# Kernel tuning notes

Measured on AMD Instinct MI355X. Metric: run time of the kernel, lower is better.

Reference implementation:

```python
import jax, jax.numpy as jnp
import numpy as np

N_HEADS = 16

def _apply_rope(x, cos, sin):
    # x: [B, S, H, D]; cos/sin: [S, D//2]
    B, S, H, D = x.shape
    half = D // 2
    x1, x2 = x[..., :half], x[..., half:]
    c = cos[:S, None, :]  # [S, 1, half] -> broadcast over heads
    s = sin[:S, None, :]
    o1 = x1 * c - x2 * s
    o2 = x1 * s + x2 * c
    return jnp.concatenate([o1, o2], axis=-1).astype(x.dtype)


def setup_inputs() -> dict:
    key = jax.random.key(0)
    ks = jax.random.split(key, 6)
    B, S, dim = 2, 2048, 2048
    head_dim = dim // N_HEADS
    half = head_dim // 2
    x = jax.random.normal(ks[0], (B, S, dim), dtype=jnp.float32)
    # real RoPE tables (theta=10000)
    inv_freq = 1.0 / (10000.0 ** (np.arange(0, half, dtype=np.float32) / half))
    t = np.arange(S, dtype=np.float32)
    freqs = np.outer(t, inv_freq)  # [S, half]
    cos = jnp.asarray(np.cos(freqs), dtype=jnp.float32)
    sin = jnp.asarray(np.sin(freqs), dtype=jnp.float32)
    scale = 0.02
    wq = jax.random.normal(ks[1], (dim, dim), dtype=jnp.float32) * scale
    wk = jax.random.normal(ks[2], (dim, dim), dtype=jnp.float32) * scale
    wv = jax.random.normal(ks[3], (dim, dim), dtype=jnp.float32) * scale
    wo = jax.random.normal(ks[4], (dim, dim), dtype=jnp.float32) * scale
    return {"x": x, "cos": cos, "sin": sin, "wq": wq, "wk": wk, "wv": wv, "wo": wo}


def reference(x, cos, sin, wq, wk, wv, wo):
    B, S, dim = x.shape
    H = N_HEADS
    Dh = dim // H
    # QKV projections (nn.Linear: x @ W.T)
    q = (x @ wq.T).reshape(B, S, H, Dh)
    k = (x @ wk.T).reshape(B, S, H, Dh)
    v = (x @ wv.T).reshape(B, S, H, Dh)
    q = _apply_rope(q, cos, sin)
    k = _apply_rope(k, cos, sin)
    # causal attention (flash_attn_func with causal=True, dropout 0 in eval)
    scores = jnp.einsum('bqhd,bkhd->bhqk', q, k) / jnp.sqrt(jnp.asarray(Dh, x.dtype))
    causal = jnp.tril(jnp.ones((S, S), dtype=bool))
    scores = jnp.where(causal, scores, jnp.asarray(-1e30, x.dtype))
    attn = jax.nn.softmax(scores, axis=-1)
    out = jnp.einsum('bhqk,bkhd->bqhd', attn, v).reshape(B, S, dim)
    return out @ wo.T
```

## Files before the change

### kernel.cpp

```cpp
#include <hip/hip_runtime.h>

typedef short short8 __attribute__((ext_vector_type(8)));
typedef float f32x4 __attribute__((ext_vector_type(4)));
typedef unsigned short ushort_t;

__device__ __forceinline__ unsigned short f2bf(float f){
  unsigned int u = __builtin_bit_cast(unsigned int, f);
  u += 0x7FFFu + ((u >> 16) & 1u);
  return (unsigned short)(u >> 16);
}
__device__ __forceinline__ float bf2f(unsigned short u){
  return __builtin_bit_cast(float, ((unsigned int)u) << 16);
}
__device__ __forceinline__ void gload_lds16(const void* g, void* l){
  __builtin_amdgcn_global_load_lds((const __attribute__((address_space(1))) unsigned int*)g,
                                   (__attribute__((address_space(3))) unsigned int*)l, 16, 0, 0);
}

__global__ __launch_bounds__(256) void cast_bf16_kernel(const float* __restrict__ in,
                                                        ushort_t* __restrict__ out, long n4){
  long i = (long)blockIdx.x*256 + threadIdx.x;
  if (i >= n4) return;
  const float4 v = reinterpret_cast<const float4*>(in)[i];
  ushort4 o; o.x=f2bf(v.x); o.y=f2bf(v.y); o.z=f2bf(v.z); o.w=f2bf(v.w);
  reinterpret_cast<ushort4*>(out)[i] = o;
}

__global__ __launch_bounds__(256) void cast4_bf16_kernel(const float* __restrict__ w0, const float* __restrict__ w1,
                                                         const float* __restrict__ w2, const float* __restrict__ w3,
                                                         ushort_t* __restrict__ o0, ushort_t* __restrict__ o1,
                                                         ushort_t* __restrict__ o2, ushort_t* __restrict__ o3,
                                                         long n4){
  long i = (long)blockIdx.x*256 + threadIdx.x;
  if (i >= n4) return;
  const float* in; ushort_t* out;
  switch (blockIdx.y){
    case 0: in = w0; out = o0; break;
    case 1: in = w1; out = o1; break;
    case 2: in = w2; out = o2; break;
    default: in = w3; out = o3; break;
  }
  const float4 v = reinterpret_cast<const float4*>(in)[i];
  ushort4 o; o.x=f2bf(v.x); o.y=f2bf(v.y); o.z=f2bf(v.z); o.w=f2bf(v.w);
  reinterpret_cast<ushort4*>(out)[i] = o;
}

__global__ __launch_bounds__(256) void rope2_kernel(ushort_t* __restrict__ Qs,
                                                    ushort_t* __restrict__ Ks,
                                                    const float* __restrict__ cosb,
                                                    const float* __restrict__ sinb){
  long idx = (long)blockIdx.x*256 + threadIdx.x;
  ushort_t* X = blockIdx.y ? Ks : Qs;
  const float scale = blockIdx.y ? 1.0f : 0.08838834764831845f;
  int dq = (int)(idx & 15);
  long rest = idx >> 4;
  int h = (int)(rest & 15); rest >>= 4;
  int s = (int)(rest & 2047);
  int b = (int)(rest >> 11);
  long base = ((long)(b*2048 + s))*2048 + h*128;
  int d0 = dq*4;
  ushort4 x1 = *(const ushort4*)&X[base + d0];
  ushort4 x2 = *(const ushort4*)&X[base + 64 + d0];
  float4 cc = *(const float4*)&cosb[s*64 + d0];
  float4 ss = *(const float4*)&sinb[s*64 + d0];
  ushort4 o1, o2;
  { float a=bf2f(x1.x), bb=bf2f(x2.x); o1.x=f2bf((a*cc.x-bb*ss.x)*scale); o2.x=f2bf((a*ss.x+bb*cc.x)*scale); }
  { float a=bf2f(x1.y), bb=bf2f(x2.y); o1.y=f2bf((a*cc.y-bb*ss.y)*scale); o2.y=f2bf((a*ss.y+bb*cc.y)*scale); }
  { float a=bf2f(x1.z), bb=bf2f(x2.z); o1.z=f2bf((a*cc.z-bb*ss.z)*scale); o2.z=f2bf((a*ss.z+bb*cc.z)*scale); }
  { float a=bf2f(x1.w), bb=bf2f(x2.w); o1.w=f2bf((a*cc.w-bb*ss.w)*scale); o2.w=f2bf((a*ss.w+bb*cc.w)*scale); }
  *(ushort4*)&X[base + d0] = o1;
  *(ushort4*)&X[base + 64 + d0] = o2;
}


#define LDA8(P, QM) do{ \
  _Pragma("unroll") for (int i_ = 0; i_ < 4; ++i_){ \
    af[i_][0] = *(const short8*)&lA[(P)*16384 + ((QM)*128 + aRowBase + i_*16)*64 + sw0]; \
    af[i_][1] = *(const short8*)&lA[(P)*16384 + ((QM)*128 + aRowBase + i_*16)*64 + sw1]; } }while(0)

#define LDB4(P, QN) do{ \
  _Pragma("unroll") for (int j_ = 0; j_ < 2; ++j_){ \
    bfr[j_][0] = *(const short8*)&lB[(P)*16384 + ((QN)*128 + bRowBase + j_*16)*64 + sw0]; \
    bfr[j_][1] = *(const short8*)&lB[(P)*16384 + ((QN)*128 + bRowBase + j_*16)*64 + sw1]; } }while(0)

#define STAGE_A(P, QM, T) do{ \
  gload_lds16(aS0 + (long)(QM)*64*K + (long)(T)*64, &lA[(P)*16384 + (QM)*8192 + tid*8]); \
  gload_lds16(aS1 + (long)(QM)*64*K + (long)(T)*64, &lA[(P)*16384 + (QM)*8192 + 4096 + tid*8]); }while(0)

#define STAGE_B(P, QN, T) do{ \
  gload_lds16(bS0 + (long)(QN)*32*K + (long)(T)*64, &lB[(P)*16384 + (QN)*8192 + tid*8]); \
  gload_lds16(bS1 + (long)(QN)*32*K + (long)(T)*64, &lB[(P)*16384 + (QN)*8192 + 4096 + tid*8]); }while(0)

#define MF16(QM, QN) do{ \
  __builtin_amdgcn_s_setprio(1); \
  _Pragma("unroll") for (int k_ = 0; k_ < 2; ++k_) \
    _Pragma("unroll") for (int i_ = 0; i_ < 4; ++i_) \
      _Pragma("unroll") for (int j_ = 0; j_ < 2; ++j_) \
        acc[(QM)*4+i_][(QN)*2+j_] = __builtin_amdgcn_mfma_f32_16x16x32_bf16(af[i_][k_], bfr[j_][k_], acc[(QM)*4+i_][(QN)*2+j_], 0, 0, 0); \
  __builtin_amdgcn_s_setprio(0); }while(0)

#define WAITC(MORE) do{ \
  if (MORE) asm volatile("s_waitcnt vmcnt(4)" ::: "memory"); \
  else      asm volatile("s_waitcnt vmcnt(0)" ::: "memory"); }while(0)

#define PH(P, QM, QN, STG, WT) do{ \
  if ((QN) == 0) { LDA8(P, QM); } \
  LDB4(P, QN); \
  STG; \
  WT; \
  __builtin_amdgcn_s_barrier(); \
  asm volatile("" ::: "memory"); \
  MF16(QM, QN); \
  __builtin_amdgcn_s_barrier(); \
  asm volatile("" ::: "memory"); }while(0)

__global__ __launch_bounds__(512, 2) void gemm_qkv_8ph(const ushort_t* __restrict__ A,
                                                       const ushort_t* __restrict__ Bw,
                                                       ushort_t* __restrict__ Cq,
                                                       ushort_t* __restrict__ Ck,
                                                       ushort_t* __restrict__ Vt,
                                                       int MT, int K){
  __shared__ ushort_t lA[32768];
  __shared__ ushort_t lB[32768];
  const int tid = threadIdx.x;
  const int lane = tid & 63, wid = tid >> 6;
  const int g = lane >> 4, c = lane & 15;
  const int wm = wid >> 2, wn = wid & 3;

  const int nwg = (int)gridDim.x, cpx = nwg >> 3;
  int sw = (blockIdx.x & 7)*cpx + (blockIdx.x >> 3);
  const long m0 = (long)(sw % MT)*256;
  const long n0 = (long)(sw / MT)*256;

  const int prl0 = tid >> 3, q1 = 512 + tid, prl1 = q1 >> 3;
  const int sl0 = ((tid & 7) ^ (prl0 & 7)) * 8;
  const int sl1 = ((q1 & 7) ^ (prl1 & 7)) * 8;
  const int rowA0 = ((prl0 >> 6)*128) + (prl0 & 63);
  const int rowA1 = ((prl1 >> 6)*128) + (prl1 & 63);
  const int rowB0 = ((prl0 >> 5)*64) + (prl0 & 31);
  const int rowB1 = ((prl1 >> 5)*64) + (prl1 & 31);
  const ushort_t* aS0 = A + (m0 + rowA0)*K + sl0;
  const ushort_t* aS1 = A + (m0 + rowA1)*K + sl1;
  const ushort_t* bS0 = Bw + (n0 + rowB0)*K + sl0;
  const ushort_t* bS1 = Bw + (n0 + rowB1)*K + sl1;

  const int sw0 = (g ^ (c & 7)) * 8;
  const int sw1 = ((4 + g) ^ (c & 7)) * 8;
  const int aRowBase = wm*64 + c;
  const int bRowBase = wn*32 + c;

  f32x4 acc[8][4] = {};
  short8 af[4][2], bfr[2][2];
  const int NI = K >> 7;

  STAGE_A(0, 0, 0); STAGE_B(0, 0, 0);
  STAGE_A(0, 1, 0); STAGE_B(0, 1, 0);
  STAGE_A(1, 0, 1); STAGE_B(1, 0, 1);
  asm volatile("s_waitcnt vmcnt(4)" ::: "memory");
  __builtin_amdgcn_s_barrier();
  asm volatile("" ::: "memory");

  for (int j = 0; j < NI; ++j){
    const int t = 2*j;
    const bool more = (j + 1 < NI);
    PH(0, 0, 0, STAGE_A(1, 1, t+1), ((void)0));
    PH(0, 0, 1, STAGE_B(1, 1, t+1), ((void)0));
    PH(0, 1, 0, if(more){STAGE_A(0, 0, t+2);}, ((void)0));
    PH(0, 1, 1, if(more){STAGE_B(0, 0, t+2);}, WAITC(more));
    PH(1, 0, 0, if(more){STAGE_A(0, 1, t+2);}, ((void)0));
    PH(1, 0, 1, if(more){STAGE_B(0, 1, t+2);}, ((void)0));
    PH(1, 1, 0, if(more){STAGE_A(1, 0, t+3);}, ((void)0));
    PH(1, 1, 1, if(more){STAGE_B(1, 0, t+3);}, WAITC(more));
  }

  const long rbase = m0 + wm*128 + g*4;
  const long cbase = n0 + wn*64 + c;
  const int third = (int)(n0 >> 11);
  if (third < 2){
    ushort_t* dst = (third == 0) ? Cq : Ck;
    const long csub = cbase - (long)third*2048;
#pragma unroll
    for (int mi = 0; mi < 8; ++mi)
#pragma unroll
      for (int ni = 0; ni < 4; ++ni){
        long off = (rbase + mi*16)*2048 + csub + ni*16;
#pragma unroll
        for (int r = 0; r < 4; ++r)
          dst[off + (long)r*2048] = f2bf(acc[mi][ni][r]);
      }
  } else {
#pragma unroll
    for (int mi = 0; mi < 8; ++mi){
      const long row = rbase + mi*16;
      const long s = row & 2047, bb = row >> 11;
#pragma unroll
      for (int ni = 0; ni < 4; ++ni){
        long hd = cbase + ni*16 - 4096;
        long vaddr = ((bb*16 + (hd >> 7))*128 + (hd & 127))*2048 + s;
        ushort4 o4;
        o4.x = f2bf(acc[mi][ni][0]); o4.y = f2bf(acc[mi][ni][1]);
        o4.z = f2bf(acc[mi][ni][2]); o4.w = f2bf(acc[mi][ni][3]);
        *(ushort4*)&Vt[vaddr] = o4;
      }
    }
  }
}

__global__ __launch_bounds__(256) void gemm_nt_lds(const ushort_t* __restrict__ A,
                                                   const ushort_t* __restrict__ B,
                                                   float* __restrict__ C,
                                                   int M, int N, int K){
  const int tid = threadIdx.x;
  const int l = tid & 63;
  const int g = l >> 4, c = l & 15;
  const int w = tid >> 6, wr = w >> 1, wc = w & 1;
  const long m0 = (long)blockIdx.x*128, n0 = (long)blockIdx.y*128;
  __shared__ ushort_t lds_a[128*32];
  __shared__ ushort_t lds_b[128*32];
  f32x4 acc[4][4] = {};
  const int q1 = tid, q2 = 256 + tid;
  const ushort_t* a1 = A + (m0 + (q1>>2))*(long)K + (q1&3)*8;
  const ushort_t* a2 = A + (m0 + (q2>>2))*(long)K + (q2&3)*8;
  const ushort_t* b1 = B + (n0 + (q1>>2))*(long)K + (q1&3)*8;
  const ushort_t* b2 = B + (n0 + (q2>>2))*(long)K + (q2&3)*8;
  for (int k0 = 0; k0 < K; k0 += 32){
    __syncthreads();
    gload_lds16(a1 + k0, &lds_a[q1*8]);
    gload_lds16(a2 + k0, &lds_a[q2*8]);
    gload_lds16(b1 + k0, &lds_b[q1*8]);
    gload_lds16(b2 + k0, &lds_b[q2*8]);
    __syncthreads();
    short8 af[4], bf[4];
#pragma unroll
    for (int i = 0; i < 4; ++i) af[i] = *(const short8*)&lds_a[(wr*64 + i*16 + c)*32 + g*8];
#pragma unroll
    for (int j = 0; j < 4; ++j) bf[j] = *(const short8*)&lds_b[(wc*64 + j*16 + c)*32 + g*8];
#pragma unroll
    for (int i = 0; i < 4; ++i)
#pragma unroll
      for (int j = 0; j < 4; ++j)
        acc[i][j] = __builtin_amdgcn_mfma_f32_16x16x32_bf16(af[i], bf[j], acc[i][j], 0, 0, 0);
  }
#pragma unroll
  for (int i = 0; i < 4; ++i)
#pragma unroll
    for (int j = 0; j < 4; ++j)
#pragma unroll
      for (int r = 0; r < 4; ++r)
        C[(m0 + wr*64 + i*16 + g*4 + r)*(long)N + n0 + wc*64 + j*16 + c] = acc[i][j][r];
}

__global__ __launch_bounds__(256) void attn_kernel(const ushort_t* __restrict__ Q,
                                                   const ushort_t* __restrict__ Kr,
                                                   const ushort_t* __restrict__ Vt,
                                                   ushort_t* __restrict__ O){
  const int tid = threadIdx.x;
  const int l = tid & 63, w = tid >> 6;
  const int g = l >> 4, c = l & 15;
  const int bh = blockIdx.x;
  const int qt = (int)gridDim.y - 1 - (int)blockIdx.y;
  const int b = bh >> 4, h = bh & 15;
  const int q0 = qt * 64;
  const int qw0 = q0 + w * 16;
  const int nt = qt + 1;

  __shared__ ushort_t k_lds[2][64*128];
  __shared__ ushort_t v_lds[2][128*64];
  __shared__ ushort_t p_lds[4][16*72];

  short8 qf[4];
  const long qbase = ((long)(b*2048 + qw0 + c))*2048 + h*128 + g*8;
#pragma unroll
  for (int ds = 0; ds < 4; ++ds) qf[ds] = *(const short8*)(Q + qbase + ds*32);

  const ushort_t* ksrc[4]; const ushort_t* vsrc[4];
  int kof[4], vof[4];
#pragma unroll
  for (int i = 0; i < 4; ++i){
    int q = i*256 + tid;
    int r = q >> 4, j = q & 15;
    ksrc[i] = Kr + ((long)(b*2048 + r))*2048 + h*128 + (j ^ (r & 7))*8;
    kof[i] = q*8;
    int d = q >> 3, jj = q & 7;
    vsrc[i] = Vt + ((long)(bh*128 + d))*2048 + (jj ^ (d & 7))*8;
    vof[i] = q*8;
  }

  f32x4 o[8] = {};
  float m = -1e30f, lsum = 0.f;
  const int sw = (c & 7) << 3;

#pragma unroll
  for (int i = 0; i < 4; ++i) gload_lds16(ksrc[i], &k_lds[0][kof[i]]);
#pragma unroll
  for (int i = 0; i < 4; ++i) gload_lds16(vsrc[i], &v_lds[0][vof[i]]);
  __syncthreads();

  for (int t = 0; t < nt; ++t){
    const int p = t & 1;
    if (t + 1 < nt){
#pragma unroll
      for (int i = 0; i < 4; ++i)
        gload_lds16(ksrc[i] + (long)(t+1)*64*2048, &k_lds[p^1][kof[i]]);
#pragma unroll
      for (int i = 0; i < 4; ++i)
        gload_lds16(vsrc[i] + (t+1)*64, &v_lds[p^1][vof[i]]);
    }
    const int kv0 = t*64;

    f32x4 s[4] = {};
    __builtin_amdgcn_s_setprio(1);
#pragma unroll
    for (int t4 = 0; t4 < 4; ++t4){
      const int row = 16*t4 + c;
#pragma unroll
      for (int ds = 0; ds < 4; ++ds){
        short8 kf = *(const short8*)&k_lds[p][(row*128 + ds*32 + g*8) ^ sw];
        s[t4] = __builtin_amdgcn_mfma_f32_16x16x32_bf16(kf, qf[ds], s[t4], 0, 0, 0);
      }
    }
    __builtin_amdgcn_s_setprio(0);
    if (kv0 + 63 > qw0){
      const int qg = qw0 + c;
#pragma unroll
      for (int t4 = 0; t4 < 4; ++t4)
#pragma unroll
        for (int r = 0; r < 4; ++r)
          if (kv0 + 16*t4 + 4*g + r > qg) s[t4][r] = -1e30f;
    }
    float tm = -1e30f;
#pragma unroll
    for (int t4 = 0; t4 < 4; ++t4)
      tm = fmaxf(tm, fmaxf(fmaxf(s[t4][0], s[t4][1]), fmaxf(s[t4][2], s[t4][3])));
    tm = fmaxf(tm, __shfl_xor(tm, 16, 64));
    tm = fmaxf(tm, __shfl_xor(tm, 32, 64));
    if (!__all(tm <= m + 8.f)){
      float mn = fmaxf(m, tm);
      float al = __expf(m - mn);
      m = mn;
      lsum *= al;
      float alr[4];
#pragma unroll
      for (int r = 0; r < 4; ++r) alr[r] = __shfl(al, 4*g + r, 64);
#pragma unroll
      for (int dt = 0; dt < 8; ++dt)
#pragma unroll
        for (int r = 0; r < 4; ++r) o[dt][r] *= alr[r];
    }
    float ps = 0.f;
#pragma unroll
    for (int t4 = 0; t4 < 4; ++t4)
#pragma unroll
      for (int r = 0; r < 4; ++r){ float pex = __expf(s[t4][r] - m); s[t4][r] = pex; ps += pex; }
    ps += __shfl_xor(ps, 16, 64);
    ps += __shfl_xor(ps, 32, 64);
    lsum += ps;
#pragma unroll
    for (int t4 = 0; t4 < 4; ++t4){
      uint2 pw;
      pw.x = (unsigned)f2bf(s[t4][0]) | ((unsigned)f2bf(s[t4][1]) << 16);
      pw.y = (unsigned)f2bf(s[t4][2]) | ((unsigned)f2bf(s[t4][3]) << 16);
      *reinterpret_cast<uint2*>(&p_lds[w][c*72 + 16*t4 + 4*g]) = pw;
    }
    __builtin_amdgcn_s_setprio(1);
#pragma unroll
    for (int kc = 0; kc < 2; ++kc){
      short8 pf = *(const short8*)&p_lds[w][c*72 + 32*kc + 8*g];
#pragma unroll
      for (int dt = 0; dt < 8; ++dt){
        short8 vf = *(const short8*)&v_lds[p][(((16*dt + c)*64) + kc*32 + g*8) ^ sw];
        o[dt] = __builtin_amdgcn_mfma_f32_16x16x32_bf16(pf, vf, o[dt], 0, 0, 0);
      }
    }
    __builtin_amdgcn_s_setprio(0);
    __syncthreads();
  }

  float inv = 1.f / lsum;
  float invr[4];
#pragma unroll
  for (int r = 0; r < 4; ++r) invr[r] = __shfl(inv, 4*g + r, 64);
  const long obase = ((long)(b*2048 + qw0 + g*4))*2048 + h*128 + c;
#pragma unroll
  for (int dt = 0; dt < 8; ++dt)
#pragma unroll
    for (int r = 0; r < 4; ++r)
      O[obase + (long)r*2048 + dt*16] = f2bf(o[dt][r] * invr[r]);
}

extern "C" void kernel_launch(void* const* d_in, const int* in_sizes, int n_in,
                              void* d_out, int out_size, void* d_ws, size_t ws_size,
                              hipStream_t stream){
  const float* x    = (const float*)d_in[0];
  const float* cosb = (const float*)d_in[1];
  const float* sinb = (const float*)d_in[2];
  const float* wq   = (const float*)d_in[3];
  const float* wk   = (const float*)d_in[4];
  const float* wv   = (const float*)d_in[5];
  const float* wo   = (const float*)d_in[6];
  float* out = (float*)d_out;

  const int S = 2048, DIM = 2048;
  const long MN = 4096;

  char* ws = (char*)d_ws;
  ushort_t* xb     = (ushort_t*)(ws);
  ushort_t* wqkvb  = (ushort_t*)(ws + (16l<<20));
  ushort_t* wob    = (ushort_t*)(ws + (40l<<20));
  ushort_t* qstage = (ushort_t*)(ws + (48l<<20));
  ushort_t* kstage = (ushort_t*)(ws + (64l<<20));
  ushort_t* attnb  = (ushort_t*)(ws + (80l<<20));
  ushort_t* vt     = (ushort_t*)(ws + (96l<<20));

  const long xn4 = MN*DIM/4, wn4 = (long)DIM*DIM/4;
  cast_bf16_kernel<<<(int)((xn4+255)/256), 256, 0, stream>>>(x, xb, xn4);
  cast4_bf16_kernel<<<dim3((int)((wn4+255)/256), 4), 256, 0, stream>>>(
      wq, wk, wv, wo,
      wqkvb, wqkvb + 4194304, wqkvb + 8388608, wob, wn4);

  gemm_qkv_8ph<<<(MN/256)*(6144/256), 512, 0, stream>>>(
      xb, wqkvb, qstage, kstage, vt, (int)(MN/256), DIM);

  const int ropeBlocks = (2*2048*16*16)/256;
  rope2_kernel<<<dim3(ropeBlocks, 2), 256, 0, stream>>>(qstage, kstage, cosb, sinb);
  attn_kernel<<<dim3(32, S/64), 256, 0, stream>>>(qstage, kstage, vt, attnb);
  gemm_nt_lds<<<dim3(MN/128, DIM/128), 256, 0, stream>>>(attnb, wob, out, (int)MN, DIM, DIM);
}
```

Before: 298.9 us.

## Reorder QKV GEMM phases by K-half to keep B fragments in registers

The 8-phase QKV GEMM loop now splits each LDS stage along the two K halves instead of along N quarters. Each wave loads all four B fragments for a K half once and reuses them across both M halves, so B fragments are no longer reloaded from LDS in every phase. The intent is to cut LDS read traffic and instruction count in the inner loop while keeping 16 MFMAs per phase and the same staging and barrier pattern. Register use shifts from A fragments to B fragments and stays about the same overall.

Result: no change. 301.0 us (+0.7%).

```diff
diff --git a/kernel.cpp b/kernel.cpp
--- a/kernel.cpp
+++ b/kernel.cpp
@@ -73,15 +73,13 @@
 }
 
 
-#define LDA8(P, QM) do{ \
-  _Pragma("unroll") for (int i_ = 0; i_ < 4; ++i_){ \
-    af[i_][0] = *(const short8*)&lA[(P)*16384 + ((QM)*128 + aRowBase + i_*16)*64 + sw0]; \
-    af[i_][1] = *(const short8*)&lA[(P)*16384 + ((QM)*128 + aRowBase + i_*16)*64 + sw1]; } }while(0)
-
-#define LDB4(P, QN) do{ \
-  _Pragma("unroll") for (int j_ = 0; j_ < 2; ++j_){ \
-    bfr[j_][0] = *(const short8*)&lB[(P)*16384 + ((QN)*128 + bRowBase + j_*16)*64 + sw0]; \
-    bfr[j_][1] = *(const short8*)&lB[(P)*16384 + ((QN)*128 + bRowBase + j_*16)*64 + sw1]; } }while(0)
+#define LDA4(P, QM, KH) do{ \
+  _Pragma("unroll") for (int i_ = 0; i_ < 4; ++i_) \
+    af[i_] = *(const short8*)&lA[(P)*16384 + ((QM)*128 + aRowBase + i_*16)*64 + ((KH)? sw1 : sw0)]; }while(0)
+
+#define LDB4K(P, KH) do{ \
+  _Pragma("unroll") for (int j_ = 0; j_ < 4; ++j_) \
+    bfr[KH][j_] = *(const short8*)&lB[(P)*16384 + (((j_>>1)*128) + bRowBase + (j_&1)*16)*64 + ((KH)? sw1 : sw0)]; }while(0)
 
 #define STAGE_A(P, QM, T) do{ \
   gload_lds16(aS0 + (long)(QM)*64*K + (long)(T)*64, &lA[(P)*16384 + (QM)*8192 + tid*8]); \
@@ -91,26 +89,24 @@
   gload_lds16(bS0 + (long)(QN)*32*K + (long)(T)*64, &lB[(P)*16384 + (QN)*8192 + tid*8]); \
   gload_lds16(bS1 + (long)(QN)*32*K + (long)(T)*64, &lB[(P)*16384 + (QN)*8192 + 4096 + tid*8]); }while(0)
 
-#define MF16(QM, QN) do{ \
+#define MFK(QM, KH) do{ \
   __builtin_amdgcn_s_setprio(1); \
-  _Pragma("unroll") for (int k_ = 0; k_ < 2; ++k_) \
-    _Pragma("unroll") for (int i_ = 0; i_ < 4; ++i_) \
-      _Pragma("unroll") for (int j_ = 0; j_ < 2; ++j_) \
-        acc[(QM)*4+i_][(QN)*2+j_] = __builtin_amdgcn_mfma_f32_16x16x32_bf16(af[i_][k_], bfr[j_][k_], acc[(QM)*4+i_][(QN)*2+j_], 0, 0, 0); \
+  _Pragma("unroll") for (int i_ = 0; i_ < 4; ++i_) \
+    _Pragma("unroll") for (int j_ = 0; j_ < 4; ++j_) \
+      acc[(QM)*4+i_][j_] = __builtin_amdgcn_mfma_f32_16x16x32_bf16(af[i_], bfr[KH][j_], acc[(QM)*4+i_][j_], 0, 0, 0); \
   __builtin_amdgcn_s_setprio(0); }while(0)
 
 #define WAITC(MORE) do{ \
   if (MORE) asm volatile("s_waitcnt vmcnt(4)" ::: "memory"); \
   else      asm volatile("s_waitcnt vmcnt(0)" ::: "memory"); }while(0)
 
-#define PH(P, QM, QN, STG, WT) do{ \
-  if ((QN) == 0) { LDA8(P, QM); } \
-  LDB4(P, QN); \
+#define PHX(RD, STG, WT, QM, KH) do{ \
+  RD; \
   STG; \
   WT; \
   __builtin_amdgcn_s_barrier(); \
   asm volatile("" ::: "memory"); \
-  MF16(QM, QN); \
+  MFK(QM, KH); \
   __builtin_amdgcn_s_barrier(); \
   asm volatile("" ::: "memory"); }while(0)
 
@@ -150,7 +146,7 @@
   const int bRowBase = wn*32 + c;
 
   f32x4 acc[8][4] = {};
-  short8 af[4][2], bfr[2][2];
+  short8 af[4], bfr[2][4];
   const int NI = K >> 7;
 
   STAGE_A(0, 0, 0); STAGE_B(0, 0, 0);
@@ -163,14 +159,14 @@
   for (int j = 0; j < NI; ++j){
     const int t = 2*j;
     const bool more = (j + 1 < NI);
-    PH(0, 0, 0, STAGE_A(1, 1, t+1), ((void)0));
-    PH(0, 0, 1, STAGE_B(1, 1, t+1), ((void)0));
-    PH(0, 1, 0, if(more){STAGE_A(0, 0, t+2);}, ((void)0));
-    PH(0, 1, 1, if(more){STAGE_B(0, 0, t+2);}, WAITC(more));
-    PH(1, 0, 0, if(more){STAGE_A(0, 1, t+2);}, ((void)0));
-    PH(1, 0, 1, if(more){STAGE_B(0, 1, t+2);}, ((void)0));
-    PH(1, 1, 0, if(more){STAGE_A(1, 0, t+3);}, ((void)0));
-    PH(1, 1, 1, if(more){STAGE_B(1, 0, t+3);}, WAITC(more));
+    PHX(LDB4K(0,0); LDA4(0,0,0), STAGE_A(1, 1, t+1),            ((void)0),   0, 0);
+    PHX(LDB4K(0,1); LDA4(0,0,1), STAGE_B(1, 1, t+1),            ((void)0),   0, 1);
+    PHX(LDA4(0,1,0),             if(more){STAGE_A(0, 0, t+2);}, ((void)0),   1, 0);
+    PHX(LDA4(0,1,1),             if(more){STAGE_B(0, 0, t+2);}, WAITC(more), 1, 1);
+    PHX(LDB4K(1,0); LDA4(1,0,0), if(more){STAGE_A(0, 1, t+2);}, ((void)0),   0, 0);
+    PHX(LDB4K(1,1); LDA4(1,0,1), if(more){STAGE_B(0, 1, t+2);}, ((void)0),   0, 1);
+    PHX(LDA4(1,1,0),             if(more){STAGE_A(1, 0, t+3);}, ((void)0),   1, 0);
+    PHX(LDA4(1,1,1),             if(more){STAGE_B(1, 0, t+3);}, WAITC(more), 1, 1);
   }
 
   const long rbase = m0 + wm*128 + g*4;
```

## Reuse B fragments across phases in QKV GEMM and peel last iteration

Applied to the files above, without the earlier changes.

The QKV GEMM's 8-phase loop now holds two A and two B register fragment sets, so B-half fragments loaded for one M-quadrant are reused for the other instead of being reloaded from LDS each phase. This cuts LDS reads per iteration. The global-to-LDS staging order is reshuffled to prefetch one more B tile in the prologue, and the final iteration is peeled to drop the runtime 'more' branches. The cost is higher register pressure from the extra fragment arrays under launch_bounds(512,2), and a retuned vmcnt wait schedule that must stay correct.

Result: faster. 283.6 us (-5.1%).

```diff
diff --git a/kernel.cpp b/kernel.cpp
--- a/kernel.cpp
+++ b/kernel.cpp
@@ -73,15 +73,15 @@
 }
 
 
-#define LDA8(P, QM) do{ \
+#define LDA8(DST, P, QM) do{ \
   _Pragma("unroll") for (int i_ = 0; i_ < 4; ++i_){ \
-    af[i_][0] = *(const short8*)&lA[(P)*16384 + ((QM)*128 + aRowBase + i_*16)*64 + sw0]; \
-    af[i_][1] = *(const short8*)&lA[(P)*16384 + ((QM)*128 + aRowBase + i_*16)*64 + sw1]; } }while(0)
-
-#define LDB4(P, QN) do{ \
+    DST[i_][0] = *(const short8*)&lA[(P)*16384 + ((QM)*128 + aRowBase + i_*16)*64 + sw0]; \
+    DST[i_][1] = *(const short8*)&lA[(P)*16384 + ((QM)*128 + aRowBase + i_*16)*64 + sw1]; } }while(0)
+
+#define LDB4(DST, P, BH) do{ \
   _Pragma("unroll") for (int j_ = 0; j_ < 2; ++j_){ \
-    bfr[j_][0] = *(const short8*)&lB[(P)*16384 + ((QN)*128 + bRowBase + j_*16)*64 + sw0]; \
-    bfr[j_][1] = *(const short8*)&lB[(P)*16384 + ((QN)*128 + bRowBase + j_*16)*64 + sw1]; } }while(0)
+    DST[j_][0] = *(const short8*)&lB[(P)*16384 + ((BH)*128 + bRowBase + j_*16)*64 + sw0]; \
+    DST[j_][1] = *(const short8*)&lB[(P)*16384 + ((BH)*128 + bRowBase + j_*16)*64 + sw1]; } }while(0)
 
 #define STAGE_A(P, QM, T) do{ \
   gload_lds16(aS0 + (long)(QM)*64*K + (long)(T)*64, &lA[(P)*16384 + (QM)*8192 + tid*8]); \
@@ -91,28 +91,16 @@
   gload_lds16(bS0 + (long)(QN)*32*K + (long)(T)*64, &lB[(P)*16384 + (QN)*8192 + tid*8]); \
   gload_lds16(bS1 + (long)(QN)*32*K + (long)(T)*64, &lB[(P)*16384 + (QN)*8192 + 4096 + tid*8]); }while(0)
 
-#define MF16(QM, QN) do{ \
+#define MFK(QM, BH, AR, BR) do{ \
   __builtin_amdgcn_s_setprio(1); \
   _Pragma("unroll") for (int k_ = 0; k_ < 2; ++k_) \
     _Pragma("unroll") for (int i_ = 0; i_ < 4; ++i_) \
       _Pragma("unroll") for (int j_ = 0; j_ < 2; ++j_) \
-        acc[(QM)*4+i_][(QN)*2+j_] = __builtin_amdgcn_mfma_f32_16x16x32_bf16(af[i_][k_], bfr[j_][k_], acc[(QM)*4+i_][(QN)*2+j_], 0, 0, 0); \
+        acc[(QM)*4+i_][(BH)*2+j_] = __builtin_amdgcn_mfma_f32_16x16x32_bf16(AR[i_][k_], BR[j_][k_], acc[(QM)*4+i_][(BH)*2+j_], 0, 0, 0); \
   __builtin_amdgcn_s_setprio(0); }while(0)
 
-#define WAITC(MORE) do{ \
-  if (MORE) asm volatile("s_waitcnt vmcnt(4)" ::: "memory"); \
-  else      asm volatile("s_waitcnt vmcnt(0)" ::: "memory"); }while(0)
-
-#define PH(P, QM, QN, STG, WT) do{ \
-  if ((QN) == 0) { LDA8(P, QM); } \
-  LDB4(P, QN); \
-  STG; \
-  WT; \
-  __builtin_amdgcn_s_barrier(); \
-  asm volatile("" ::: "memory"); \
-  MF16(QM, QN); \
-  __builtin_amdgcn_s_barrier(); \
-  asm volatile("" ::: "memory"); }while(0)
+#define BAR() do{ __builtin_amdgcn_s_barrier(); asm volatile("" ::: "memory"); }while(0)
+#define VM(N) asm volatile("s_waitcnt vmcnt(" #N ")" ::: "memory")
 
 __global__ __launch_bounds__(512, 2) void gemm_qkv_8ph(const ushort_t* __restrict__ A,
                                                        const ushort_t* __restrict__ Bw,
@@ -150,27 +138,36 @@
   const int bRowBase = wn*32 + c;
 
   f32x4 acc[8][4] = {};
-  short8 af[4][2], bfr[2][2];
+  short8 aR[4][2], aR2[4][2], b0[2][2], b1[2][2];
   const int NI = K >> 7;
 
   STAGE_A(0, 0, 0); STAGE_B(0, 0, 0);
-  STAGE_A(0, 1, 0); STAGE_B(0, 1, 0);
-  STAGE_A(1, 0, 1); STAGE_B(1, 0, 1);
-  asm volatile("s_waitcnt vmcnt(4)" ::: "memory");
-  __builtin_amdgcn_s_barrier();
-  asm volatile("" ::: "memory");
-
-  for (int j = 0; j < NI; ++j){
+  STAGE_B(0, 1, 0); STAGE_A(0, 1, 0);
+  STAGE_A(1, 0, 1); STAGE_B(1, 0, 1); STAGE_B(1, 1, 1);
+  VM(6);
+  BAR();
+
+  for (int j = 0; j < NI-1; ++j){
     const int t = 2*j;
-    const bool more = (j + 1 < NI);
-    PH(0, 0, 0, STAGE_A(1, 1, t+1), ((void)0));
-    PH(0, 0, 1, STAGE_B(1, 1, t+1), ((void)0));
-    PH(0, 1, 0, if(more){STAGE_A(0, 0, t+2);}, ((void)0));
-    PH(0, 1, 1, if(more){STAGE_B(0, 0, t+2);}, WAITC(more));
-    PH(1, 0, 0, if(more){STAGE_A(0, 1, t+2);}, ((void)0));
-    PH(1, 0, 1, if(more){STAGE_B(0, 1, t+2);}, ((void)0));
-    PH(1, 1, 0, if(more){STAGE_A(1, 0, t+3);}, ((void)0));
-    PH(1, 1, 1, if(more){STAGE_B(1, 0, t+3);}, WAITC(more));
+     LDA8(aR, 0, 0); LDB4(b0, 0, 0); STAGE_A(1, 1, t+1); BAR(); MFK(0, 0, aR, b0); BAR();
+     LDB4(b1, 0, 1);                 STAGE_A(0, 0, t+2); BAR(); MFK(0, 1, aR, b1); BAR();
+     LDA8(aR2, 0, 1);                STAGE_B(0, 0, t+2); BAR(); MFK(1, 0, aR2, b0); BAR();
+     VM(4);                          STAGE_B(0, 1, t+2); BAR(); MFK(1, 1, aR2, b1); BAR();
+     LDA8(aR, 1, 0); LDB4(b0, 1, 0); STAGE_A(0, 1, t+2); BAR(); MFK(0, 0, aR, b0); BAR();
+     LDB4(b1, 1, 1);                 STAGE_A(1, 0, t+3); BAR(); MFK(0, 1, aR, b1); BAR();
+     LDA8(aR2, 1, 1);                STAGE_B(1, 0, t+3); BAR(); MFK(1, 0, aR2, b0); BAR();
+     VM(4);                          STAGE_B(1, 1, t+3); BAR(); MFK(1, 1, aR2, b1); BAR();
+  }
+  {
+    const int t = 2*(NI-1);
+     LDA8(aR, 0, 0); LDB4(b0, 0, 0); STAGE_A(1, 1, t+1); BAR(); MFK(0, 0, aR, b0); BAR();
+     LDB4(b1, 0, 1);                                     BAR(); MFK(0, 1, aR, b1); BAR();
+     LDA8(aR2, 0, 1);                                    BAR(); MFK(1, 0, aR2, b0); BAR();
+     VM(0);                                              BAR(); MFK(1, 1, aR2, b1); BAR();
+     LDA8(aR, 1, 0); LDB4(b0, 1, 0);                     BAR(); MFK(0, 0, aR, b0); BAR();
+     LDB4(b1, 1, 1);                                     BAR(); MFK(0, 1, aR, b1); BAR();
+     LDA8(aR2, 1, 1);                                    BAR(); MFK(1, 0, aR2, b0); BAR();
+                                                         BAR(); MFK(1, 1, aR2, b1); BAR();
   }
 
   const long rbase = m0 + wm*128 + g*4;
```
